# Kernel optimization log

Measured on AMD Instinct MI355X. Metric: run time of the kernel, lower is better.

The kernel has to match this reference:

```python
import jax, jax.numpy as jnp
import numpy as np

N, E, D = 50000, 400000, 64
L, NA, NS = 5, 4, 3            # layers, num aggregators, num scalers
ATOM_C, ATOM_V = 9, 64         # OGB-style atom feature columns / vocab
BOND_C, BOND_V = 3, 8
EPS = 1e-5
AVG_LOG = float(np.log(9.0))   # avg_d['log'] = ln(avg_degree + 1), avg_degree = 8


def setup_inputs() -> dict:
    key = jax.random.key(0)
    ks = jax.random.split(key, 8)
    x = jax.random.randint(ks[0], (N, ATOM_C), 0, ATOM_V)
    edge_index = jax.random.randint(ks[1], (2, E), 0, N)
    edge_attr = jax.random.randint(ks[2], (E, BOND_C), 0, BOND_V)
    init = lambda k, shape, fan: (jax.random.normal(k, shape, jnp.float32) / np.sqrt(fan))
    atom_emb = init(ks[3], (ATOM_C, ATOM_V, D), D)
    bond_emb = init(ks[4], (BOND_C, BOND_V, D), D)
    pre_W = init(ks[5], (L, 3 * D, D), 3 * D)                 # pretrans: Linear(3D -> D)
    pre_b = jnp.zeros((L, D), jnp.float32)
    post_W = init(ks[6], (L, (NA * NS + 1) * D, D), (NA * NS + 1) * D)  # posttrans: Linear(13D -> D)
    post_b = jnp.zeros((L, D), jnp.float32)
    return dict(x=x, edge_index=edge_index, edge_attr=edge_attr,
                atom_emb=atom_emb, bond_emb=bond_emb,
                pre_W=pre_W, pre_b=pre_b, post_W=post_W, post_b=post_b)


def reference(x, edge_index, edge_attr, atom_emb, bond_emb, pre_W, pre_b, post_W, post_b):
    src, dst = edge_index[0], edge_index[1]  # PyG: x_j = x[edge_index[0]], x_i = x[edge_index[1]]
    # Encoders: sum of per-column categorical embeddings (OGB Atom/BondEncoder)
    h0 = atom_emb[jnp.arange(ATOM_C)[None, :], x].sum(axis=1)        # [N, D]
    e = bond_emb[jnp.arange(BOND_C)[None, :], edge_attr].sum(axis=1)  # [E, D]
    # message input cat([x_i, x_j, edge_attr]) -- identical for every layer since
    # PNAGNN.forward never feeds layer output back in as x (faithful to source)
    z2 = jnp.concatenate([h0[dst], h0[src], e], axis=-1)              # [E, 3D]
    deg = jax.ops.segment_sum(jnp.ones((E,), jnp.float32), dst, num_segments=N)
    degc = jnp.maximum(deg, 1.0)[:, None]
    log_deg = jnp.log(jnp.maximum(deg, 1.0) + 1.0)[:, None]           # guard deg=0 for attenuation
    amp = log_deg / AVG_LOG
    att = AVG_LOG / log_deg
    has = (deg > 0)[:, None]
    h_in = h0
    for l in range(L):
        m = z2 @ pre_W[l] + pre_b[l]                                  # pretrans (1 layer, no act)
        s_sum = jax.ops.segment_sum(m, dst, num_segments=N)
        mean = s_sum / degc
        mx = jnp.where(has, jax.ops.segment_max(m, dst, num_segments=N), 0.0)
        mn = jnp.where(has, jax.ops.segment_min(m, dst, num_segments=N), 0.0)
        mean_sq = jax.ops.segment_sum(m * m, dst, num_segments=N) / degc
        var = jax.nn.relu(mean_sq - mean * mean)
        std = jnp.sqrt(var + EPS)
        agg = jnp.concatenate([mean, mx, mn, std], axis=-1)           # [N, 4D]
        scaled = jnp.concatenate([agg, agg * amp, agg * att], axis=-1)  # [N, 12D]
        hcat = jnp.concatenate([scaled, h0], axis=-1)                 # [N, 13D]
        out = hcat @ post_W[l] + post_b[l]                            # posttrans (1 layer, no act)
        h = out + h_in                                                # PNAGNN residual
        h_in = h
    return h
```

## Files before the change

### kernel.cpp

```cpp
#include <hip/hip_runtime.h>
#include <hip/hip_bf16.h>

#define NN 50000
#define NE 400000
#define AVG_LOG_F 2.1972245773362196f
#define EPSV 1e-5f

typedef __hip_bfloat16 bf16;
typedef __attribute__((ext_vector_type(8))) short short8v;
typedef __attribute__((ext_vector_type(4))) float f32x4;
typedef __attribute__((ext_vector_type(2))) _Float16 h2v;

__device__ __forceinline__ float b2f(bf16 v){ return __bfloat162float(v); }
__device__ __forceinline__ bf16  f2b(float v){ return __float2bfloat16(v); }
__device__ __forceinline__ short f2s(float v){
  bf16 b = __float2bfloat16(v);
  short s; __builtin_memcpy(&s, &b, 2); return s;
}
__device__ __forceinline__ short f2h(float v){
  _Float16 h = (_Float16)v;
  short s; __builtin_memcpy(&s, &h, 2); return s;
}

__global__ void k_h0(const int* __restrict__ x, const float* __restrict__ aemb,
                     bf16* __restrict__ h0b){
  int idx = blockIdx.x * 256 + threadIdx.x;
  if (idx >= NN * 64) return;
  int n = idx >> 6, d = idx & 63;
  float acc = 0.f;
  #pragma unroll
  for (int c = 0; c < 9; ++c){
    int a = x[n * 9 + c];
    acc += aemb[(c * 64 + a) * 64 + d];
  }
  h0b[idx] = f2b(acc);
}

__global__ void k_deg_code(const int* __restrict__ ei, const int* __restrict__ ea,
                           int* __restrict__ deg, int* __restrict__ code){
  int e = blockIdx.x * 256 + threadIdx.x;
  if (e >= NE) return;
  int dst = ei[NE + e];
  atomicAdd(&deg[dst], 1);
  code[e] = ea[e * 3] + 8 * ea[e * 3 + 1] + 64 * ea[e * 3 + 2];
}

__global__ void k_scan1(const int* __restrict__ deg, int* __restrict__ rowptr,
                        int* __restrict__ part){
  __shared__ int s[256];
  int t = threadIdx.x, i = blockIdx.x * 256 + t;
  int v = (i < NN) ? deg[i] : 0;
  s[t] = v; __syncthreads();
  for (int off = 1; off < 256; off <<= 1){
    int xv = (t >= off) ? s[t - off] : 0;
    __syncthreads();
    s[t] += xv;
    __syncthreads();
  }
  if (i < NN) rowptr[i] = s[t] - v;
  if (t == 255) part[blockIdx.x] = s[255];
}

__global__ void k_scan2(int* __restrict__ part, int nblk){
  __shared__ int s[256];
  int t = threadIdx.x;
  int v = (t < nblk) ? part[t] : 0;
  s[t] = v; __syncthreads();
  for (int off = 1; off < 256; off <<= 1){
    int xv = (t >= off) ? s[t - off] : 0;
    __syncthreads();
    s[t] += xv;
    __syncthreads();
  }
  if (t < nblk) part[t] = s[t] - v;
}

__global__ void k_scan3(int* __restrict__ rowptr, const int* __restrict__ part,
                        const int* __restrict__ deg, float* __restrict__ amp,
                        float* __restrict__ att){
  int i = blockIdx.x * 256 + threadIdx.x;
  if (i < NN){
    rowptr[i] += part[blockIdx.x];
    int d = deg[i];
    float ld = logf((float)max(d, 1) + 1.0f);
    amp[i] = ld / AVG_LOG_F;
    att[i] = AVG_LOG_F / ld;
  }
  if (i == 0) rowptr[NN] = NE;
}

__global__ void k_scatter(const int* __restrict__ ei, const int* __restrict__ code,
                          const int* __restrict__ rowptr, int* __restrict__ cursor,
                          int2* __restrict__ sedge){
  int e = blockIdx.x * 256 + threadIdx.x;
  if (e >= NE) return;
  int dst = ei[NE + e];
  int pos = rowptr[dst] + atomicAdd(&cursor[dst], 1);
  int2 v; v.x = ei[e] * 1280; v.y = code[e] * 640;
  sedge[pos] = v;
}

__global__ void k_ctab(const float* __restrict__ bemb, const float* __restrict__ preW,
                       _Float16* __restrict__ CTp){
  __shared__ float et[64];
  int cb = blockIdx.x, l = blockIdx.y, t = threadIdx.x;
  int a0 = cb & 7, a1 = (cb >> 3) & 7, a2 = (cb >> 6) & 7;
  et[t] = bemb[(0 * 8 + a0) * 64 + t] + bemb[(1 * 8 + a1) * 64 + t] + bemb[(2 * 8 + a2) * 64 + t];
  __syncthreads();
  float acc = 0.f;
  const float* W = preW + (l * 192 + 128) * 64;
  for (int k = 0; k < 64; ++k) acc += et[k] * W[k * 64 + t];
  char* base = (char*)CTp + (size_t)cb * 640;
  if (l < 4) *(short*)(base + t * 8 + l * 2) = f2h(acc);
  else       *(short*)(base + 512 + t * 2)   = f2h(acc);
}

__global__ void k_whsum(const float* __restrict__ postW, const float* __restrict__ postb,
                        float* __restrict__ whs, float* __restrict__ bs){
  int idx = blockIdx.x * 256 + threadIdx.x;
  if (idx < 4096){
    int k = idx >> 6, d = idx & 63;
    float a = 0.f;
    for (int l = 0; l < 5; ++l) a += postW[(size_t)(l * 832 + 768 + k) * 64 + d];
    whs[idx] = a;
  }
  if (idx < 64){
    float a = 0.f;
    for (int l = 0; l < 5; ++l) a += postb[l * 64 + idx];
    bs[idx] = a;
  }
}

__global__ void k_wtk(const float* __restrict__ postW, bf16* __restrict__ WtKf){
  int idx = blockIdx.x * 256 + threadIdx.x;
  if (idx >= 40 * 12 * 64 * 8) return;
  int s   = idx / 6144;
  int rem = idx % 6144;
  int gw  = rem / 512;
  int lane = (rem % 512) / 8;
  int j   = idx & 7;
  int g = gw >> 2, w4 = gw & 3;
  int kp = s * 32 + (lane >> 4) * 8 + j;
  int l = kp >> 8, kl = kp & 255;
  int c = w4 * 16 + (lane & 15);
  WtKf[idx] = f2b(postW[((size_t)l * 832 + g * 256 + kl) * 64 + c]);
}

__global__ void k_wtpre896(const float* __restrict__ preW, const float* __restrict__ preb,
                           const float* __restrict__ whs, const float* __restrict__ bs,
                           bf16* __restrict__ Wtp, float* __restrict__ bias896){
  int idx = blockIdx.x * 256 + threadIdx.x;
  if (idx < 896 * 64){
    int gc = idx >> 6, k = idx & 63;
    float v;
    if (gc < 320){
      int l = gc >> 6, c = gc & 63;
      v = preW[(size_t)(l * 192 + k) * 64 + c];
    } else if (gc < 832){
      int q = gc - 320, d = q >> 3, l = q & 7;
      v = (l < 5) ? preW[(size_t)(l * 192 + 64 + k) * 64 + d] : 0.f;
    } else {
      int c = gc - 832;
      v = whs[k * 64 + c] + ((k == c) ? 1.f : 0.f);
    }
    Wtp[idx] = f2b(v);
  }
  if (idx < 896){
    float b;
    if (idx < 320)      b = preb[(idx >> 6) * 64 + (idx & 63)];
    else if (idx < 832) b = 0.f;
    else                b = bs[idx - 832];
    bias896[idx] = b;
  }
}

__global__ __launch_bounds__(256) void k_ab_mfma(const bf16* __restrict__ h0b,
                                                 const bf16* __restrict__ Wtp,
                                                 const float* __restrict__ bias896,
                                                 char* __restrict__ ABU,
                                                 float* __restrict__ out){
  __shared__ bf16 As[128][72];
  __shared__ bf16 Bs[128][72];
  const int t = threadIdx.x;
  const int n0 = blockIdx.x * 128;
  const int gc0 = blockIdx.y * 128;
  const int lane = t & 63, wid = t >> 6;
  const int rw = wid * 32;
  const short* H  = (const short*)h0b;
  const short* Wp = (const short*)Wtp;

  #pragma unroll
  for (int i = 0; i < 4; ++i){
    int idx = t + i * 256;
    int r = idx >> 3, ko = (idx & 7) * 8;
    int n = n0 + r;
    short8v v = short8v{0,0,0,0,0,0,0,0};
    if (n < NN) v = *(const short8v*)(H + (size_t)n * 64 + ko);
    *(short8v*)&As[r][ko] = v;
  }
  #pragma unroll
  for (int i = 0; i < 4; ++i){
    int idx = t + i * 256;
    int cc = idx >> 3, ko = (idx & 7) * 8;
    *(short8v*)&Bs[cc][ko] = *(const short8v*)(Wp + (size_t)(gc0 + cc) * 64 + ko);
  }
  __syncthreads();

  f32x4 acc[2][8] = {};
  #pragma unroll
  for (int kk = 0; kk < 2; ++kk){
    short8v af0 = *(const short8v*)&As[rw + (lane & 15)][kk * 32 + (lane >> 4) * 8];
    short8v af1 = *(const short8v*)&As[rw + 16 + (lane & 15)][kk * 32 + (lane >> 4) * 8];
    #pragma unroll
    for (int j = 0; j < 8; ++j){
      short8v bfj = *(const short8v*)&Bs[j * 16 + (lane & 15)][kk * 32 + (lane >> 4) * 8];
      acc[0][j] = __builtin_amdgcn_mfma_f32_16x16x32_bf16(af0, bfj, acc[0][j], 0, 0, 0);
      acc[1][j] = __builtin_amdgcn_mfma_f32_16x16x32_bf16(af1, bfj, acc[1][j], 0, 0, 0);
    }
  }

  #pragma unroll
  for (int i = 0; i < 2; ++i){
    #pragma unroll
    for (int r = 0; r < 4; ++r){
      int n = n0 + rw + i * 16 + (lane >> 4) * 4 + r;
      if (n >= NN) continue;
      char* nb = ABU + (size_t)n * 1280;
      #pragma unroll
      for (int j = 0; j < 8; ++j){
        int gc = gc0 + j * 16 + (lane & 15);
        float v = acc[i][j][r] + bias896[gc];
        if (gc < 320){
          *(short*)(nb + gc * 2) = f2h(v);
        } else if (gc < 832){
          int q = gc - 320, dd = q >> 3, l = q & 7;
          if (l < 4)       *(short*)(nb + 640 + dd * 8 + l * 2) = f2h(v);
          else if (l == 4) *(short*)(nb + 1152 + dd * 2)        = f2h(v);
        } else {
          out[(size_t)n * 64 + (gc - 832)] = v;
        }
      }
    }
  }
}

__global__ __launch_bounds__(1024, 8) void k_gather(const char* __restrict__ ABU,
                                                    const char* __restrict__ CTp,
                                                    const int* __restrict__ rowptr,
                                                    const int2* __restrict__ sedge,
                                                    bf16* __restrict__ AGGf){
  __shared__ __align__(16) short ag[16][1288];
  const int t = threadIdx.x, lane = t & 63, wid = t >> 6;
  const int n = blockIdx.x * 16 + wid;
  const char* AB8 = ABU + 640;
  const char* AB2 = ABU + 1152;
  const char* CT8 = CTp;
  const char* CT2 = CTp + 512;

  int r0 = rowptr[n], r1 = rowptr[n + 1];
  float s[5]  = {0.f, 0.f, 0.f, 0.f, 0.f};
  float sq[5] = {0.f, 0.f, 0.f, 0.f, 0.f};
  const _Float16 FLO = (_Float16)(-65504.f);
  const _Float16 FHI = (_Float16)( 65504.f);
  h2v mx01 = h2v{FLO, FLO}, mx23 = h2v{FLO, FLO};
  h2v mn01 = h2v{FHI, FHI}, mn23 = h2v{FHI, FHI};
  float mx4 = -65504.f, mn4 = 65504.f;

  union U8 { uint2 u; h2v h[2]; };
  const int l8 = lane * 8, l2 = lane * 2;

  for (int j = r0; j < r1; j += 4){
    int rem = r1 - j;
    int2 e0 = sedge[j];
    int2 e1 = (rem > 1) ? sedge[j + 1] : e0;
    int2 e2 = (rem > 2) ? sedge[j + 2] : e0;
    int2 e3 = (rem > 3) ? sedge[j + 3] : e0;
    U8 a0, a1, a2, a3, c0, c1, c2, c3;
    unsigned short b0, b1, b2, b3, d0, d1, d2, d3;
    a0.u = *(const uint2*)(AB8 + e0.x + l8);  b0 = *(const unsigned short*)(AB2 + e0.x + l2);
    c0.u = *(const uint2*)(CT8 + e0.y + l8);  d0 = *(const unsigned short*)(CT2 + e0.y + l2);
    a1.u = *(const uint2*)(AB8 + e1.x + l8);  b1 = *(const unsigned short*)(AB2 + e1.x + l2);
    c1.u = *(const uint2*)(CT8 + e1.y + l8);  d1 = *(const unsigned short*)(CT2 + e1.y + l2);
    a2.u = *(const uint2*)(AB8 + e2.x + l8);  b2 = *(const unsigned short*)(AB2 + e2.x + l2);
    c2.u = *(const uint2*)(CT8 + e2.y + l8);  d2 = *(const unsigned short*)(CT2 + e2.y + l2);
    a3.u = *(const uint2*)(AB8 + e3.x + l8);  b3 = *(const unsigned short*)(AB2 + e3.x + l2);
    c3.u = *(const uint2*)(CT8 + e3.y + l8);  d3 = *(const unsigned short*)(CT2 + e3.y + l2);

    #define EDGE_ACC(A, C, BL, DL) {                                \
      h2v t01 = A.h[0] + C.h[0];                                    \
      h2v t23 = A.h[1] + C.h[1];                                    \
      _Float16 hb, hd;                                              \
      __builtin_memcpy(&hb, &BL, 2);                                \
      __builtin_memcpy(&hd, &DL, 2);                                \
      float f4 = (float)(hb + hd);                                  \
      mx01 = __builtin_elementwise_max(mx01, t01);                  \
      mx23 = __builtin_elementwise_max(mx23, t23);                  \
      mn01 = __builtin_elementwise_min(mn01, t01);                  \
      mn23 = __builtin_elementwise_min(mn23, t23);                  \
      mx4 = fmaxf(mx4, f4); mn4 = fminf(mn4, f4);                   \
      float f0 = (float)t01[0], f1 = (float)t01[1];                 \
      float f2 = (float)t23[0], f3 = (float)t23[1];                 \
      s[0] += f0; sq[0] = fmaf(f0, f0, sq[0]);                      \
      s[1] += f1; sq[1] = fmaf(f1, f1, sq[1]);                      \
      s[2] += f2; sq[2] = fmaf(f2, f2, sq[2]);                      \
      s[3] += f3; sq[3] = fmaf(f3, f3, sq[3]);                      \
      s[4] += f4; sq[4] = fmaf(f4, f4, sq[4]);                      \
    }
    EDGE_ACC(a0, c0, b0, d0);
    if (rem > 1) EDGE_ACC(a1, c1, b1, d1);
    if (rem > 2) EDGE_ACC(a2, c2, b2, d2);
    if (rem > 3) EDGE_ACC(a3, c3, b3, d3);
    #undef EDGE_ACC
  }

  float mx[5] = {(float)mx01[0], (float)mx01[1], (float)mx23[0], (float)mx23[1], mx4};
  float mn[5] = {(float)mn01[0], (float)mn01[1], (float)mn23[0], (float)mn23[1], mn4};

  int d = r1 - r0;
  float degc = (float)((d > 0) ? d : 1);
  const char* nb = ABU + (size_t)n * 1280;
  #pragma unroll
  for (int l = 0; l < 5; ++l){
    _Float16 Kh; __builtin_memcpy(&Kh, nb + l * 128 + lane * 2, 2);
    float K = (float)Kh;
    float mean = ((float)d * K + s[l]) / degc;
    float MX = (d > 0) ? (K + mx[l]) : 0.f;
    float MN = (d > 0) ? (K + mn[l]) : 0.f;
    float mu = s[l] / degc;
    float var = fmaxf(sq[l] / degc - mu * mu, 0.f);
    float sd = sqrtf(var + EPSV);
    ag[wid][l * 256 + lane]       = f2s(mean);
    ag[wid][l * 256 + 64 + lane]  = f2s(MX);
    ag[wid][l * 256 + 128 + lane] = f2s(MN);
    ag[wid][l * 256 + 192 + lane] = f2s(sd);
  }
  __syncthreads();

  char* dst = (char*)AGGf + (size_t)blockIdx.x * 40960;
  for (int c = t; c < 2560; c += 1024){
    int ln = c & 63;
    int row = ln & 15;
    int k = (c >> 6) * 32 + (ln >> 4) * 8;
    short8v v = *(const short8v*)&ag[row][k];
    *(short8v*)(dst + (size_t)c * 16) = v;
  }
}

__global__ __launch_bounds__(256, 2) void k_post5(const bf16* __restrict__ AGGf,
                                                  const bf16* __restrict__ WtKf,
                                                  const float* __restrict__ amp,
                                                  const float* __restrict__ att,
                                                  float* __restrict__ out){
  const int t = threadIdx.x, lane = t & 63, w4 = t >> 6;
  const long g0 = (long)blockIdx.x * 4;
  const char* pa = (const char*)AGGf + (size_t)g0 * 40960 + lane * 16;
  const char* pb = (const char*)WtKf + w4 * 1024 + lane * 16;

  f32x4 acc[4][3] = {};
  short8v Ax[4], Bx[3], Ay[4], By[3];

  #define LOADX(sidx) { \
    _Pragma("unroll") for (int gi = 0; gi < 4; ++gi) \
      Ax[gi] = *(const short8v*)(pa + (size_t)gi * 40960 + (size_t)(sidx) * 1024); \
    _Pragma("unroll") for (int g = 0; g < 3; ++g) \
      Bx[g] = *(const short8v*)(pb + (size_t)(sidx) * 12288 + g * 4096); }
  #define LOADY(sidx) { \
    _Pragma("unroll") for (int gi = 0; gi < 4; ++gi) \
      Ay[gi] = *(const short8v*)(pa + (size_t)gi * 40960 + (size_t)(sidx) * 1024); \
    _Pragma("unroll") for (int g = 0; g < 3; ++g) \
      By[g] = *(const short8v*)(pb + (size_t)(sidx) * 12288 + g * 4096); }
  #define MFMAX { \
    _Pragma("unroll") for (int gi = 0; gi < 4; ++gi){ \
      _Pragma("unroll") for (int g = 0; g < 3; ++g) \
        acc[gi][g] = __builtin_amdgcn_mfma_f32_16x16x32_bf16(Ax[gi], Bx[g], acc[gi][g], 0, 0, 0); } }
  #define MFMAY { \
    _Pragma("unroll") for (int gi = 0; gi < 4; ++gi){ \
      _Pragma("unroll") for (int g = 0; g < 3; ++g) \
        acc[gi][g] = __builtin_amdgcn_mfma_f32_16x16x32_bf16(Ay[gi], By[g], acc[gi][g], 0, 0, 0); } }

  LOADX(0);
  LOADY(1);
  for (int k = 0; k < 19; ++k){
    MFMAX;
    LOADX(2 * k + 2);
    MFMAY;
    LOADY(2 * k + 3);
  }
  MFMAX;
  MFMAY;
  #undef LOADX
  #undef LOADY
  #undef MFMAX
  #undef MFMAY

  #pragma unroll
  for (int gi = 0; gi < 4; ++gi){
    #pragma unroll
    for (int r = 0; r < 4; ++r){
      long n = (g0 + gi) * 16 + (lane >> 4) * 4 + r;
      if (n >= NN) continue;
      float am = amp[n], at = att[n];
      int c = w4 * 16 + (lane & 15);
      out[(size_t)n * 64 + c] += acc[gi][0][r] + am * acc[gi][1][r] + at * acc[gi][2][r];
    }
  }
}

extern "C" void kernel_launch(void* const* d_in, const int* in_sizes, int n_in,
                              void* d_out, int out_size, void* d_ws, size_t ws_size,
                              hipStream_t stream){
  const int*   x     = (const int*)d_in[0];
  const int*   ei    = (const int*)d_in[1];
  const int*   ea    = (const int*)d_in[2];
  const float* aemb  = (const float*)d_in[3];
  const float* bemb  = (const float*)d_in[4];
  const float* preW  = (const float*)d_in[5];
  const float* preb  = (const float*)d_in[6];
  const float* postW = (const float*)d_in[7];
  const float* postb = (const float*)d_in[8];
  float* out = (float*)d_out;

  char* p = (char*)d_ws;
  auto alloc = [&](size_t bytes) -> char* {
    char* r = p;
    p += (bytes + 255) & ~(size_t)255;
    return r;
  };
  bf16*      h0b     = (bf16*)     alloc((size_t)NN * 64 * 2);
  char*      ABU     = (char*)     alloc((size_t)NN * 1280);
  bf16*      AGGf    = (bf16*)     alloc((size_t)3128 * 40960);
  int*       deg     = (int*)      alloc((size_t)NN * 4);
  int*       rowptr  = (int*)      alloc((size_t)(NN + 1) * 4);
  int*       cursor  = (int*)      alloc((size_t)NN * 4);
  float*     amp     = (float*)    alloc((size_t)NN * 4);
  float*     att     = (float*)    alloc((size_t)NN * 4);
  int*       code    = (int*)      alloc((size_t)NE * 4);
  int2*      sedge   = (int2*)     alloc((size_t)NE * 8);
  _Float16*  CTp     = (_Float16*) alloc((size_t)512 * 640);
  float*     whs     = (float*)    alloc((size_t)64 * 64 * 4);
  float*     bs      = (float*)    alloc((size_t)64 * 4);
  int*       part    = (int*)      alloc((size_t)256 * 4);
  bf16*      WtKf    = (bf16*)     alloc((size_t)40 * 12 * 64 * 8 * 2);
  bf16*      Wtp     = (bf16*)     alloc((size_t)896 * 64 * 2);
  float*     bias896 = (float*)    alloc((size_t)896 * 4);
  if ((size_t)(p - (char*)d_ws) > ws_size) return;

  hipMemsetAsync(deg, 0, (size_t)NN * 4, stream);
  hipMemsetAsync(cursor, 0, (size_t)NN * 4, stream);

  k_h0<<<dim3((NN * 64 + 255) / 256), 256, 0, stream>>>(x, aemb, h0b);
  k_deg_code<<<dim3((NE + 255) / 256), 256, 0, stream>>>(ei, ea, deg, code);
  int nblk = (NN + 255) / 256;
  k_scan1<<<dim3(nblk), 256, 0, stream>>>(deg, rowptr, part);
  k_scan2<<<dim3(1), 256, 0, stream>>>(part, nblk);
  k_scan3<<<dim3(nblk), 256, 0, stream>>>(rowptr, part, deg, amp, att);
  k_scatter<<<dim3((NE + 255) / 256), 256, 0, stream>>>(ei, code, rowptr, cursor, sedge);
  k_ctab<<<dim3(512, 5), 64, 0, stream>>>(bemb, preW, CTp);
  k_whsum<<<dim3(16), 256, 0, stream>>>(postW, postb, whs, bs);
  k_wtk<<<dim3((40 * 12 * 64 * 8 + 255) / 256), 256, 0, stream>>>(postW, WtKf);
  k_wtpre896<<<dim3((896 * 64 + 255) / 256), 256, 0, stream>>>(preW, preb, whs, bs,
                                                               Wtp, bias896);
  k_ab_mfma<<<dim3((NN + 127) / 128, 7), 256, 0, stream>>>(h0b, Wtp, bias896, ABU, out);
  k_gather<<<dim3(NN / 16), 1024, 0, stream>>>(ABU, (const char*)CTp, rowptr, sedge, AGGf);
  k_post5<<<dim3(782), 256, 0, stream>>>(AGGf, WtKf, amp, att, out);
}
```

Before: 277.4 us.

## Fuse post-transform MFMA GEMM into gather kernel and inline weight-sum prep

The post-transform GEMM (k_post5) is folded into the gather kernel. After the aggregates are built in shared memory, four waves of each block run the 16x1280 by 1280x192 MFMA directly from LDS, so the large AGGf intermediate no longer makes a round trip through global memory. The separate k_whsum kernel is also removed and its weight and bias sums are computed inline in k_wtpre896, saving one launch. In exchange, only 4 of the 16 waves do the GEMM while the rest idle, each block streams the whole WtKf weight set from cache, and the launch bound minimum drops from 8 to 2 blocks.

```diff
diff --git a/kernel.cpp b/kernel.cpp
--- a/kernel.cpp
+++ b/kernel.cpp
@@ -115,22 +115,6 @@
   else       *(short*)(base + 512 + t * 2)   = f2h(acc);
 }
 
-__global__ void k_whsum(const float* __restrict__ postW, const float* __restrict__ postb,
-                        float* __restrict__ whs, float* __restrict__ bs){
-  int idx = blockIdx.x * 256 + threadIdx.x;
-  if (idx < 4096){
-    int k = idx >> 6, d = idx & 63;
-    float a = 0.f;
-    for (int l = 0; l < 5; ++l) a += postW[(size_t)(l * 832 + 768 + k) * 64 + d];
-    whs[idx] = a;
-  }
-  if (idx < 64){
-    float a = 0.f;
-    for (int l = 0; l < 5; ++l) a += postb[l * 64 + idx];
-    bs[idx] = a;
-  }
-}
-
 __global__ void k_wtk(const float* __restrict__ postW, bf16* __restrict__ WtKf){
   int idx = blockIdx.x * 256 + threadIdx.x;
   if (idx >= 40 * 12 * 64 * 8) return;
@@ -147,7 +131,7 @@
 }
 
 __global__ void k_wtpre896(const float* __restrict__ preW, const float* __restrict__ preb,
-                           const float* __restrict__ whs, const float* __restrict__ bs,
+                           const float* __restrict__ postW, const float* __restrict__ postb,
                            bf16* __restrict__ Wtp, float* __restrict__ bias896){
   int idx = blockIdx.x * 256 + threadIdx.x;
   if (idx < 896 * 64){
@@ -161,7 +145,10 @@
       v = (l < 5) ? preW[(size_t)(l * 192 + 64 + k) * 64 + d] : 0.f;
     } else {
       int c = gc - 832;
-      v = whs[k * 64 + c] + ((k == c) ? 1.f : 0.f);
+      float a = 0.f;
+      #pragma unroll
+      for (int l = 0; l < 5; ++l) a += postW[(size_t)(l * 832 + 768 + k) * 64 + c];
+      v = a + ((k == c) ? 1.f : 0.f);
     }
     Wtp[idx] = f2b(v);
   }
@@ -169,7 +156,12 @@
     float b;
     if (idx < 320)      b = preb[(idx >> 6) * 64 + (idx & 63)];
     else if (idx < 832) b = 0.f;
-    else                b = bs[idx - 832];
+    else {
+      float a = 0.f;
+      #pragma unroll
+      for (int l = 0; l < 5; ++l) a += postb[l * 64 + (idx - 832)];
+      b = a;
+    }
     bias896[idx] = b;
   }
 }
@@ -244,11 +236,14 @@
   }
 }
 
-__global__ __launch_bounds__(1024, 8) void k_gather(const char* __restrict__ ABU,
+__global__ __launch_bounds__(1024, 2) void k_gather(const char* __restrict__ ABU,
                                                     const char* __restrict__ CTp,
                                                     const int* __restrict__ rowptr,
                                                     const int2* __restrict__ sedge,
-                                                    bf16* __restrict__ AGGf){
+                                                    const bf16* __restrict__ WtKf,
+                                                    const float* __restrict__ amp,
+                                                    const float* __restrict__ att,
+                                                    float* __restrict__ out){
   __shared__ __align__(16) short ag[16][1288];
   const int t = threadIdx.x, lane = t & 63, wid = t >> 6;
   const int n = blockIdx.x * 16 + wid;
@@ -336,73 +331,46 @@
   }
   __syncthreads();
 
-  char* dst = (char*)AGGf + (size_t)blockIdx.x * 40960;
-  for (int c = t; c < 2560; c += 1024){
-    int ln = c & 63;
-    int row = ln & 15;
-    int k = (c >> 6) * 32 + (ln >> 4) * 8;
-    short8v v = *(const short8v*)&ag[row][k];
-    *(short8v*)(dst + (size_t)c * 16) = v;
-  }
-}
-
-__global__ __launch_bounds__(256, 2) void k_post5(const bf16* __restrict__ AGGf,
-                                                  const bf16* __restrict__ WtKf,
-                                                  const float* __restrict__ amp,
-                                                  const float* __restrict__ att,
-                                                  float* __restrict__ out){
-  const int t = threadIdx.x, lane = t & 63, w4 = t >> 6;
-  const long g0 = (long)blockIdx.x * 4;
-  const char* pa = (const char*)AGGf + (size_t)g0 * 40960 + lane * 16;
-  const char* pb = (const char*)WtKf + w4 * 1024 + lane * 16;
-
-  f32x4 acc[4][3] = {};
-  short8v Ax[4], Bx[3], Ay[4], By[3];
-
-  #define LOADX(sidx) { \
-    _Pragma("unroll") for (int gi = 0; gi < 4; ++gi) \
-      Ax[gi] = *(const short8v*)(pa + (size_t)gi * 40960 + (size_t)(sidx) * 1024); \
+  if (wid >= 4) return;
+
+  const char* pb = (const char*)WtKf + wid * 1024 + lane * 16;
+  const short* agrow = &ag[lane & 15][(lane >> 4) * 8];
+  f32x4 acc[3] = {};
+  short8v Bx[3], By[3];
+
+  #define LOADB(dst, sidx) { \
     _Pragma("unroll") for (int g = 0; g < 3; ++g) \
-      Bx[g] = *(const short8v*)(pb + (size_t)(sidx) * 12288 + g * 4096); }
-  #define LOADY(sidx) { \
-    _Pragma("unroll") for (int gi = 0; gi < 4; ++gi) \
-      Ay[gi] = *(const short8v*)(pa + (size_t)gi * 40960 + (size_t)(sidx) * 1024); \
+      dst[g] = *(const short8v*)(pb + (size_t)(sidx) * 12288 + g * 4096); }
+  #define MFMA3(af, B) { \
     _Pragma("unroll") for (int g = 0; g < 3; ++g) \
-      By[g] = *(const short8v*)(pb + (size_t)(sidx) * 12288 + g * 4096); }
-  #define MFMAX { \
-    _Pragma("unroll") for (int gi = 0; gi < 4; ++gi){ \
-      _Pragma("unroll") for (int g = 0; g < 3; ++g) \
-        acc[gi][g] = __builtin_amdgcn_mfma_f32_16x16x32_bf16(Ax[gi], Bx[g], acc[gi][g], 0, 0, 0); } }
-  #define MFMAY { \
-    _Pragma("unroll") for (int gi = 0; gi < 4; ++gi){ \
-      _Pragma("unroll") for (int g = 0; g < 3; ++g) \
-        acc[gi][g] = __builtin_amdgcn_mfma_f32_16x16x32_bf16(Ay[gi], By[g], acc[gi][g], 0, 0, 0); } }
-
-  LOADX(0);
-  LOADY(1);
+      acc[g] = __builtin_amdgcn_mfma_f32_16x16x32_bf16(af, B[g], acc[g], 0, 0, 0); }
+
+  LOADB(Bx, 0);
   for (int k = 0; k < 19; ++k){
-    MFMAX;
-    LOADX(2 * k + 2);
-    MFMAY;
-    LOADY(2 * k + 3);
-  }
-  MFMAX;
-  MFMAY;
-  #undef LOADX
-  #undef LOADY
-  #undef MFMAX
-  #undef MFMAY
-
-  #pragma unroll
-  for (int gi = 0; gi < 4; ++gi){
-    #pragma unroll
-    for (int r = 0; r < 4; ++r){
-      long n = (g0 + gi) * 16 + (lane >> 4) * 4 + r;
-      if (n >= NN) continue;
-      float am = amp[n], at = att[n];
-      int c = w4 * 16 + (lane & 15);
-      out[(size_t)n * 64 + c] += acc[gi][0][r] + am * acc[gi][1][r] + at * acc[gi][2][r];
-    }
+    LOADB(By, 2 * k + 1);
+    short8v af0 = *(const short8v*)(agrow + (2 * k) * 32);
+    MFMA3(af0, Bx);
+    LOADB(Bx, 2 * k + 2);
+    short8v af1 = *(const short8v*)(agrow + (2 * k + 1) * 32);
+    MFMA3(af1, By);
+  }
+  LOADB(By, 39);
+  {
+    short8v af0 = *(const short8v*)(agrow + 38 * 32);
+    MFMA3(af0, Bx);
+    short8v af1 = *(const short8v*)(agrow + 39 * 32);
+    MFMA3(af1, By);
+  }
+  #undef LOADB
+  #undef MFMA3
+
+  #pragma unroll
+  for (int r = 0; r < 4; ++r){
+    int row = (lane >> 4) * 4 + r;
+    int nn = blockIdx.x * 16 + row;
+    float am = amp[nn], at = att[nn];
+    int c = wid * 16 + (lane & 15);
+    out[(size_t)nn * 64 + c] += acc[0][r] + am * acc[1][r] + at * acc[2][r];
   }
 }
 
@@ -428,7 +396,6 @@
   };
   bf16*      h0b     = (bf16*)     alloc((size_t)NN * 64 * 2);
   char*      ABU     = (char*)     alloc((size_t)NN * 1280);
-  bf16*      AGGf    = (bf16*)     alloc((size_t)3128 * 40960);
   int*       deg     = (int*)      alloc((size_t)NN * 4);
   int*       rowptr  = (int*)      alloc((size_t)(NN + 1) * 4);
   int*       cursor  = (int*)      alloc((size_t)NN * 4);
@@ -437,8 +404,6 @@
   int*       code    = (int*)      alloc((size_t)NE * 4);
   int2*      sedge   = (int2*)     alloc((size_t)NE * 8);
   _Float16*  CTp     = (_Float16*) alloc((size_t)512 * 640);
-  float*     whs     = (float*)    alloc((size_t)64 * 64 * 4);
-  float*     bs      = (float*)    alloc((size_t)64 * 4);
   int*       part    = (int*)      alloc((size_t)256 * 4);
   bf16*      WtKf    = (bf16*)     alloc((size_t)40 * 12 * 64 * 8 * 2);
   bf16*      Wtp     = (bf16*)     alloc((size_t)896 * 64 * 2);
@@ -456,11 +421,10 @@
   k_scan3<<<dim3(nblk), 256, 0, stream>>>(rowptr, part, deg, amp, att);
   k_scatter<<<dim3((NE + 255) / 256), 256, 0, stream>>>(ei, code, rowptr, cursor, sedge);
   k_ctab<<<dim3(512, 5), 64, 0, stream>>>(bemb, preW, CTp);
-  k_whsum<<<dim3(16), 256, 0, stream>>>(postW, postb, whs, bs);
   k_wtk<<<dim3((40 * 12 * 64 * 8 + 255) / 256), 256, 0, stream>>>(postW, WtKf);
-  k_wtpre896<<<dim3((896 * 64 + 255) / 256), 256, 0, stream>>>(preW, preb, whs, bs,
+  k_wtpre896<<<dim3((896 * 64 + 255) / 256), 256, 0, stream>>>(preW, preb, postW, postb,
                                                                Wtp, bias896);
   k_ab_mfma<<<dim3((NN + 127) / 128, 7), 256, 0, stream>>>(h0b, Wtp, bias896, ABU, out);
-  k_gather<<<dim3(NN / 16), 1024, 0, stream>>>(ABU, (const char*)CTp, rowptr, sedge, AGGf);
-  k_post5<<<dim3(782), 256, 0, stream>>>(AGGf, WtKf, amp, att, out);
-}
+  k_gather<<<dim3(NN / 16), 1024, 0, stream>>>(ABU, (const char*)CTp, rowptr, sedge,
+                                               WtKf, amp, att, out);
+}
```

New measurement: 267.6 us. -3.5%, faster.
